# Kernel tuning notes

Measured on AMD Instinct MI355X. Metric: run time of the kernel, lower is better.

The kernel has to match this reference:

```python
import jax, jax.numpy as jnp
import numpy as np

NUM_ATOM_TYPES = 28   # ZINC-Full atom vocab
HIDDEN_DIM = 128
N_ATOMS = 500_000
N_INCIDENCES = 2_000_000
NUM_CYCLES = 500_000  # static segment count for scatter_sum output


def setup_inputs() -> dict:
    key = jax.random.key(0)
    k1, k2, k3 = jax.random.split(key, 3)
    x = jax.random.randint(k1, (N_ATOMS,), 0, NUM_ATOM_TYPES, dtype=jnp.int64)
    atom_to_cycle = jax.random.randint(
        k2, (2, N_INCIDENCES), 0, NUM_CYCLES, dtype=jnp.int64)
    # row 0 must index into x's N_ATOMS rows; NUM_CYCLES == N_ATOMS so in-range.
    emb_weight = jax.random.normal(k3, (NUM_ATOM_TYPES, HIDDEN_DIM), dtype=jnp.float32)
    return {"x": x, "atom_to_cycle": atom_to_cycle, "emb_weight": emb_weight}


def reference(x, atom_to_cycle, emb_weight):
    # Embedding lookup: [N_ATOMS, H]
    h = emb_weight[x]
    # Gather per-incidence atom embeddings: [E, H]
    gathered = h[atom_to_cycle[0]]
    # scatter_sum over cycle ids -> [NUM_CYCLES, H]
    return jax.ops.segment_sum(gathered, atom_to_cycle[1], num_segments=NUM_CYCLES)
```

## Files before the change

kernel.cpp:

```cpp
#include <hip/hip_runtime.h>
#include <string.h>

#define H 128
#define NTYPES 28
#define CNT_BYTES_PER_CYCLE 32

typedef float f32x4 __attribute__((ext_vector_type(4)));

__global__ void count_kernel(const int* __restrict__ a2c,
                             const int* __restrict__ x,
                             unsigned* __restrict__ cnt,
                             int n_inc) {
    int i = (blockIdx.x * blockDim.x + threadIdx.x) * 4;
    if (i + 3 < n_inc) {
        int4 at = *(const int4*)(a2c + i);
        int4 cy = *(const int4*)(a2c + n_inc + i);
        int t0 = x[at.x], t1 = x[at.y], t2 = x[at.z], t3 = x[at.w];
        atomicAdd(&cnt[cy.x * 8 + (t0 >> 2)], 1u << (8 * (t0 & 3)));
        atomicAdd(&cnt[cy.y * 8 + (t1 >> 2)], 1u << (8 * (t1 & 3)));
        atomicAdd(&cnt[cy.z * 8 + (t2 >> 2)], 1u << (8 * (t2 & 3)));
        atomicAdd(&cnt[cy.w * 8 + (t3 >> 2)], 1u << (8 * (t3 & 3)));
    } else {
        for (int e = i; e < n_inc; ++e) {
            int atom = a2c[e];
            int cycv = a2c[n_inc + e];
            int t = x[atom];
            atomicAdd(&cnt[cycv * 8 + (t >> 2)], 1u << (8 * (t & 3)));
        }
    }
}

__global__ __launch_bounds__(256) void expand2_kernel(
        const unsigned char* __restrict__ cnt,
        const float* __restrict__ emb,
        float* __restrict__ out,
        int num_cycles) {
    __shared__ __align__(16) float lds[NTYPES * H];
    for (int i = threadIdx.x; i < NTYPES * H; i += blockDim.x) lds[i] = emb[i];
    __syncthreads();
    const f32x4* l4 = (const f32x4*)lds;

    const int lane = threadIdx.x & 63;
    const int half = lane >> 5;
    const int hl   = lane & 31;
    const int w    = blockIdx.x * (blockDim.x >> 6) + (threadIdx.x >> 6);
    const int nw   = gridDim.x * (blockDim.x >> 6);

    const int P   = (num_cycles + 1) >> 1;
    const int ppw = (P + nw - 1) / nw;
    int p0 = w * ppw;
    int p1 = p0 + ppw; if (p1 > P) p1 = P;
    if (p0 >= p1) return;

    unsigned b0 = cnt[(size_t)p0 * 64 + lane];
    unsigned b1 = (p0 + 1 < p1) ? cnt[(size_t)(p0 + 1) * 64 + lane] : 0u;

    for (int p = p0; p < p1; ++p) {
        unsigned b = b0;
        b0 = b1;
        b1 = (p + 2 < p1) ? cnt[(size_t)(p + 2) * 64 + lane] : 0u;

        int c = 2 * p + half;
        unsigned long long bal = __ballot(b != 0);
        unsigned m = (half ? (unsigned)(bal >> 32) : (unsigned)bal) & 0x0FFFFFFFu;
        if (c >= num_cycles) m = 0;

        f32x4 acc = {0.f, 0.f, 0.f, 0.f};
        while (m) {
            int t = __builtin_ctz(m);
            m &= m - 1;
            float f = (float)(unsigned)__shfl((int)b, t + (half << 5));
            f32x4 wv = l4[t * 32 + hl];
            acc += f * wv;
        }
        if (c < num_cycles) {
            f32x4* dst = (f32x4*)(out + (size_t)c * H) + hl;
            *dst = acc;
        }
    }
}

__global__ void scatter_direct_kernel(const int* __restrict__ a2c,
                                      const int* __restrict__ x,
                                      const float* __restrict__ emb,
                                      float* __restrict__ out,
                                      int n_inc) {
    int gid = blockIdx.x * blockDim.x + threadIdx.x;
    int e  = gid >> 5;
    int ch = gid & 31;
    if (e >= n_inc) return;
    int atom = a2c[e];
    int cyc  = a2c[n_inc + e];
    int t    = x[atom];
    const float4 w = ((const float4*)(emb + t * H))[ch];
    float* o = out + (size_t)cyc * H + ch * 4;
    atomicAdd(o + 0, w.x);
    atomicAdd(o + 1, w.y);
    atomicAdd(o + 2, w.z);
    atomicAdd(o + 3, w.w);
}

__global__ void zero_u4_kernel(uint4* __restrict__ p, int n4) {
    int i = blockIdx.x * blockDim.x + threadIdx.x;
    if (i < n4) p[i] = make_uint4(0u, 0u, 0u, 0u);
}

extern "C" void kernel_launch(void* const* d_in, const int* in_sizes, int n_in,
                              void* d_out, int out_size, void* d_ws, size_t ws_size,
                              hipStream_t stream) {
    const int*   x    = (const int*)d_in[0];
    const int*   a2c  = (const int*)d_in[1];
    const float* emb  = (const float*)d_in[2];
    float*       out  = (float*)d_out;

    const int n_inc      = in_sizes[1] / 2;
    const int num_cycles = out_size / H;
    const size_t cnt_bytes = (size_t)num_cycles * CNT_BYTES_PER_CYCLE;

    if (ws_size >= cnt_bytes) {
        unsigned* cnt = (unsigned*)d_ws;
        hipMemsetAsync(d_ws, 0, cnt_bytes, stream);
        int nthreads = (n_inc + 3) / 4;
        count_kernel<<<(nthreads + 255) / 256, 256, 0, stream>>>(a2c, x, cnt, n_inc);
        expand2_kernel<<<2048, 256, 0, stream>>>(
            (const unsigned char*)cnt, emb, out, num_cycles);
    } else {
        int n4 = out_size / 4;
        zero_u4_kernel<<<(n4 + 255) / 256, 256, 0, stream>>>((uint4*)d_out, n4);
        long long total = (long long)n_inc * 32;
        int blocks = (int)((total + 255) / 256);
        scatter_direct_kernel<<<blocks, 256, 0, stream>>>(a2c, x, emb, out, n_inc);
    }
}
```

Measured before the change: 368.4 us.

## Bucket incidences by cycle range and build type histograms in LDS

Replaces the global-atomic count pass and its memset with a two-stage radix-style partition. Incidences are first bucketed by cycle-id high bits into a packed key array. Each bucket is then histogrammed in shared memory and written out densely. The intent is to replace scattered global atomics with LDS atomics and coalesced writes. The cost is an extra key write and read pass, and the histogram stage launches only about 245 blocks.

```diff
diff --git a/kernel.cpp b/kernel.cpp
--- a/kernel.cpp
+++ b/kernel.cpp
@@ -5,7 +5,131 @@
 #define NTYPES 28
 #define CNT_BYTES_PER_CYCLE 32
 
+#define SHIFT 11
+#define MAXB  256
+#define CHUNK 8192
+
 typedef float f32x4 __attribute__((ext_vector_type(4)));
+
+__global__ __launch_bounds__(256) void partition_kernel(
+        const int* __restrict__ a2c, const int* __restrict__ x,
+        unsigned* __restrict__ keys,
+        unsigned* __restrict__ tstart, unsigned* __restrict__ tlen,
+        int n_inc, int nbkt) {
+    __shared__ unsigned hcnt[MAXB];
+    __shared__ unsigned hoff[MAXB];
+    const int tid  = threadIdx.x;
+    const int base = blockIdx.x * CHUNK;
+    const int lim  = min(base + CHUNK, n_inc);
+
+    hcnt[tid] = 0;
+    __syncthreads();
+
+    for (int q = 0; q < CHUNK / 1024; ++q) {
+        int off = base + q * 1024 + tid * 4;
+        if (off + 3 < lim) {
+            int4 cy = *(const int4*)(a2c + n_inc + off);
+            atomicAdd(&hcnt[(unsigned)cy.x >> SHIFT], 1u);
+            atomicAdd(&hcnt[(unsigned)cy.y >> SHIFT], 1u);
+            atomicAdd(&hcnt[(unsigned)cy.z >> SHIFT], 1u);
+            atomicAdd(&hcnt[(unsigned)cy.w >> SHIFT], 1u);
+        } else {
+            for (int e = off; e < lim && e < off + 4; ++e)
+                atomicAdd(&hcnt[(unsigned)a2c[n_inc + e] >> SHIFT], 1u);
+        }
+    }
+    __syncthreads();
+
+    unsigned v = hcnt[tid];
+    hoff[tid] = v;
+    __syncthreads();
+    for (int d = 1; d < MAXB; d <<= 1) {
+        unsigned u = (tid >= d) ? hoff[tid - d] : 0u;
+        __syncthreads();
+        hoff[tid] += u;
+        __syncthreads();
+    }
+    unsigned excl = hoff[tid] - v;
+
+    if (tid < nbkt) {
+        tstart[tid * MAXB + blockIdx.x] = (unsigned)base + excl;
+        tlen  [tid * MAXB + blockIdx.x] = v;
+    }
+    hoff[tid] = (unsigned)base + excl;
+    __syncthreads();
+
+    for (int q = 0; q < CHUNK / 1024; ++q) {
+        int off = base + q * 1024 + tid * 4;
+        if (off + 3 < lim) {
+            int4 at = *(const int4*)(a2c + off);
+            int4 cy = *(const int4*)(a2c + n_inc + off);
+            int t0 = x[at.x], t1 = x[at.y], t2 = x[at.z], t3 = x[at.w];
+            unsigned p;
+            p = atomicAdd(&hoff[(unsigned)cy.x >> SHIFT], 1u);
+            keys[p] = ((unsigned)cy.x << 5) | (unsigned)t0;
+            p = atomicAdd(&hoff[(unsigned)cy.y >> SHIFT], 1u);
+            keys[p] = ((unsigned)cy.y << 5) | (unsigned)t1;
+            p = atomicAdd(&hoff[(unsigned)cy.z >> SHIFT], 1u);
+            keys[p] = ((unsigned)cy.z << 5) | (unsigned)t2;
+            p = atomicAdd(&hoff[(unsigned)cy.w >> SHIFT], 1u);
+            keys[p] = ((unsigned)cy.w << 5) | (unsigned)t3;
+        } else {
+            for (int e = off; e < lim && e < off + 4; ++e) {
+                unsigned key = ((unsigned)a2c[n_inc + e] << 5)
+                             | (unsigned)x[a2c[e]];
+                unsigned p = atomicAdd(&hoff[key >> (5 + SHIFT)], 1u);
+                keys[p] = key;
+            }
+        }
+    }
+}
+
+__global__ __launch_bounds__(256) void bucket_hist_kernel(
+        const unsigned* __restrict__ keys,
+        const unsigned* __restrict__ tstart, const unsigned* __restrict__ tlen,
+        unsigned* __restrict__ cnt, int num_cycles, int nblk1) {
+    __shared__ unsigned hist[(1 << SHIFT) * 8];
+    __shared__ unsigned rstart[MAXB];
+    __shared__ unsigned rexcl[MAXB];
+    __shared__ unsigned plen[MAXB];
+    const int tid = threadIdx.x;
+    const int b   = blockIdx.x;
+
+    for (int k = tid; k < (1 << SHIFT) * 8; k += 256) hist[k] = 0;
+    unsigned L = (tid < nblk1) ? tlen[b * MAXB + tid] : 0u;
+    rstart[tid] = (tid < nblk1) ? tstart[b * MAXB + tid] : 0u;
+    plen[tid] = L;
+    __syncthreads();
+    for (int d = 1; d < MAXB; d <<= 1) {
+        unsigned u = (tid >= d) ? plen[tid - d] : 0u;
+        __syncthreads();
+        plen[tid] += u;
+        __syncthreads();
+    }
+    rexcl[tid] = plen[tid] - L;
+    __syncthreads();
+    const unsigned T = plen[MAXB - 1];
+
+    for (unsigned g = tid; g < T; g += 256) {
+        int lo = 0, hi = MAXB - 1;
+        while (lo < hi) {
+            int mid = (lo + hi) >> 1;
+            if (plen[mid] > g) hi = mid; else lo = mid + 1;
+        }
+        unsigned key = keys[rstart[lo] + (g - rexcl[lo])];
+        unsigned lc  = (key >> 5) & ((1u << SHIFT) - 1u);
+        unsigned t   = key & 31u;
+        atomicAdd(&hist[lc * 8 + (t >> 2)], 1u << (8 * (t & 3)));
+    }
+    __syncthreads();
+
+    const int cb  = b << SHIFT;
+    int ncyc = num_cycles - cb;
+    if (ncyc > (1 << SHIFT)) ncyc = 1 << SHIFT;
+    const int ndw = ncyc * 8;
+    for (int k = tid; k < ndw; k += 256)
+        cnt[(size_t)cb * 8 + k] = hist[k];
+}
 
 __global__ void count_kernel(const int* __restrict__ a2c,
                              const int* __restrict__ x,
@@ -22,10 +146,8 @@
         atomicAdd(&cnt[cy.w * 8 + (t3 >> 2)], 1u << (8 * (t3 & 3)));
     } else {
         for (int e = i; e < n_inc; ++e) {
-            int atom = a2c[e];
-            int cycv = a2c[n_inc + e];
-            int t = x[atom];
-            atomicAdd(&cnt[cycv * 8 + (t >> 2)], 1u << (8 * (t & 3)));
+            int t = x[a2c[e]];
+            atomicAdd(&cnt[a2c[n_inc + e] * 8 + (t >> 2)], 1u << (8 * (t & 3)));
         }
     }
 }
@@ -89,9 +211,8 @@
     int e  = gid >> 5;
     int ch = gid & 31;
     if (e >= n_inc) return;
-    int atom = a2c[e];
-    int cyc  = a2c[n_inc + e];
-    int t    = x[atom];
+    int t = x[a2c[e]];
+    int cyc = a2c[n_inc + e];
     const float4 w = ((const float4*)(emb + t * H))[ch];
     float* o = out + (size_t)cyc * H + ch * 4;
     atomicAdd(o + 0, w.x);
@@ -117,7 +238,28 @@
     const int num_cycles = out_size / H;
     const size_t cnt_bytes = (size_t)num_cycles * CNT_BYTES_PER_CYCLE;
 
-    if (ws_size >= cnt_bytes) {
+    const int nbkt  = (num_cycles > 0) ? (((num_cycles - 1) >> SHIFT) + 1) : 0;
+    const int nblk1 = (n_inc + CHUNK - 1) / CHUNK;
+    const size_t keys_bytes = ((size_t)n_inc * 4 + 255) & ~(size_t)255;
+    const size_t tab_bytes  = 2 * (size_t)MAXB * MAXB * 4;
+    const size_t cnt_off    = (keys_bytes + tab_bytes + 255) & ~(size_t)255;
+    const size_t need_part  = cnt_off + cnt_bytes;
+
+    if (num_cycles > 0 && n_inc > 0 && nbkt <= MAXB && nblk1 <= MAXB &&
+        ws_size >= need_part) {
+        char* wsb = (char*)d_ws;
+        unsigned* keys   = (unsigned*)wsb;
+        unsigned* tstart = (unsigned*)(wsb + keys_bytes);
+        unsigned* tlen   = tstart + (size_t)MAXB * MAXB;
+        unsigned* cnt    = (unsigned*)(wsb + cnt_off);
+
+        partition_kernel<<<nblk1, 256, 0, stream>>>(
+            a2c, x, keys, tstart, tlen, n_inc, nbkt);
+        bucket_hist_kernel<<<nbkt, 256, 0, stream>>>(
+            keys, tstart, tlen, cnt, num_cycles, nblk1);
+        expand2_kernel<<<2048, 256, 0, stream>>>(
+            (const unsigned char*)cnt, emb, out, num_cycles);
+    } else if (ws_size >= cnt_bytes) {
         unsigned* cnt = (unsigned*)d_ws;
         hipMemsetAsync(d_ws, 0, cnt_bytes, stream);
         int nthreads = (n_inc + 3) / 4;
```

Measured after the change: 351.7 us. 4.5% less time.
